# Performance work log

Hardware: AMD Instinct MI355X
Metric: run time of the kernel (lower is better)

## Reference

```python
import jax, jax.numpy as jnp
import numpy as np

# Synthetic layered DAG: 8 node-layers of width N -> 7 masked dense layers.
B = 4096        # batch
N = 2048        # nodes per DAG layer (= in_features = out_features)
DEPTH = 7       # number of weight layers (len(L) - 1)
DENSITY = 0.25  # fraction of predecessor edges present (mask sparsity)


def setup_inputs() -> dict:
    key = jax.random.key(0)
    kx, kw, km = jax.random.split(key, 3)
    x = jax.random.normal(kx, (B, N), dtype=jnp.float32)
    # Mask M: [DEPTH, N+1, N]; random 0/1 edges, last row (bias) all ones.
    m = (jax.random.uniform(km, (DEPTH, N + 1, N)) < DENSITY).astype(jnp.float32)
    M = m.at[:, -1, :].set(1.0)
    # Kaiming-uniform per column: bound = 1/sqrt(nnz_j) (torch code's init),
    # nonzero only at masked positions (W initialized to zeros elsewhere).
    nnz = jnp.maximum(M.sum(axis=1, keepdims=True), 1.0)  # [DEPTH,1,N]
    u = jax.random.uniform(kw, (DEPTH, N + 1, N), minval=-1.0, maxval=1.0)
    W = (u / jnp.sqrt(nnz)) * M
    return {"x": x, "W": W, "M": M}


def reference(x, W, M):
    # activations buffer semantics collapse to a per-layer chain because each
    # layer's preds are exactly the previous DAG layer; sinks = last layer.
    def step(acts, wm):
        w, m = wm  # [N+1, N] each
        h = jnp.concatenate(
            [acts, jnp.ones((acts.shape[0], 1), acts.dtype)], axis=1)  # [B, N+1]
        acts = jax.nn.relu(h @ (m * w))  # masked dense matmul + ReLU
        return acts, None

    out, _ = jax.lax.scan(step, x, (W, M))
    return out  # [B, N] activations of sink nodes
```

## Files before the change

### kernel.cpp

```cpp
#include <hip/hip_runtime.h>
#include <hip/hip_bf16.h>

typedef __bf16 bf16_t;
typedef __bf16 v8bf __attribute__((ext_vector_type(8)));
typedef __bf16 v4bf __attribute__((ext_vector_type(4)));
typedef float  v4f  __attribute__((ext_vector_type(4)));

#define B_ROWS 4096
#define N_COLS 2048
#define K_FULL 2049
#define K_PAD  2112
#define DEPTH  7

#define BM 128
#define BN 128
#define BK 64
#define NT (K_PAD / BK)

__global__ __launch_bounds__(256) void wt_kernel(const float* __restrict__ W,
                                                 bf16_t* __restrict__ Wt) {
  __shared__ float t[64][65];
  const int l  = blockIdx.z;
  const int k0 = blockIdx.x * 64;
  const int n0 = blockIdx.y * 64;
  const int tid = threadIdx.x;
  const int r  = tid >> 4;
  const int c4 = (tid & 15) * 4;
  const float* Wl = W + (size_t)l * K_FULL * N_COLS;
#pragma unroll
  for (int it = 0; it < 4; ++it) {
    const int k = k0 + r + it * 16;
    float4 v = make_float4(0.f, 0.f, 0.f, 0.f);
    if (k < K_FULL) v = *(const float4*)&Wl[(size_t)k * N_COLS + n0 + c4];
    t[c4 + 0][r + it * 16] = v.x;
    t[c4 + 1][r + it * 16] = v.y;
    t[c4 + 2][r + it * 16] = v.z;
    t[c4 + 3][r + it * 16] = v.w;
  }
  __syncthreads();
  bf16_t* Wtl = Wt + (size_t)l * N_COLS * K_PAD;
#pragma unroll
  for (int it = 0; it < 4; ++it) {
    const int n = r + it * 16;
    v4bf o;
    o[0] = (bf16_t)t[n][c4 + 0];
    o[1] = (bf16_t)t[n][c4 + 1];
    o[2] = (bf16_t)t[n][c4 + 2];
    o[3] = (bf16_t)t[n][c4 + 3];
    *(v4bf*)&Wtl[(size_t)(n0 + n) * K_PAD + k0 + c4] = o;
  }
}

__global__ __launch_bounds__(256) void init_kernel(const float* __restrict__ x,
                                                   bf16_t* __restrict__ A0,
                                                   bf16_t* __restrict__ A1) {
  const int c4 = (blockIdx.x * 256 + threadIdx.x) * 4;
  const int r  = blockIdx.y;
  if (c4 >= K_PAD) return;
  v4bf o;
  if (c4 < N_COLS) {
    const float4 v = *(const float4*)&x[(size_t)r * N_COLS + c4];
    o[0] = (bf16_t)v.x; o[1] = (bf16_t)v.y; o[2] = (bf16_t)v.z; o[3] = (bf16_t)v.w;
  } else {
    o[0] = (bf16_t)(c4 == N_COLS ? 1.0f : 0.0f);
    o[1] = (bf16_t)0.0f; o[2] = (bf16_t)0.0f; o[3] = (bf16_t)0.0f;
  }
  *(v4bf*)&A0[(size_t)r * K_PAD + c4] = o;
  if (c4 >= N_COLS) *(v4bf*)&A1[(size_t)r * K_PAD + c4] = o;
}

__global__ __launch_bounds__(512, 4) void gemm_kernel(
    const bf16_t* __restrict__ A, const bf16_t* __restrict__ Bt,
    bf16_t* __restrict__ Cn, float* __restrict__ Co) {
  __shared__ __align__(16) bf16_t As[BM * BK];
  __shared__ __align__(16) bf16_t Bs[BN * BK];

  const int tid  = threadIdx.x;
  const int wave = tid >> 6;
  const int lane = tid & 63;
  const int m0 = blockIdx.y * BM;
  const int n0 = blockIdx.x * BN;
  const int wm = (wave & 1) * 64;
  const int wn = (wave >> 1) * 32;
  const int quad = lane >> 4;
  const int l16  = lane & 15;

  int srow[2], scol[2];
#pragma unroll
  for (int c = 0; c < 2; ++c) {
    const int gran = wave * 128 + c * 64 + lane;
    srow[c] = gran >> 3;
    scol[c] = ((gran & 7) ^ (srow[c] & 7)) << 3;
  }
  const size_t aoff[2] = {(size_t)(m0 + srow[0]) * K_PAD + scol[0],
                          (size_t)(m0 + srow[1]) * K_PAD + scol[1]};
  const size_t boff[2] = {(size_t)(n0 + srow[0]) * K_PAD + scol[0],
                          (size_t)(n0 + srow[1]) * K_PAD + scol[1]};

  v4f acc[4][2] = {};

  for (int kt = 0; kt < NT; ++kt) {
    const int kbase = kt * BK;
    __syncthreads();
#pragma unroll
    for (int c = 0; c < 2; ++c) {
      __builtin_amdgcn_global_load_lds(
          (const __attribute__((address_space(1))) void*)(A + aoff[c] + kbase),
          (__attribute__((address_space(3))) void*)((char*)As + wave * 2048 + c * 1024),
          16, 0, 0);
    }
#pragma unroll
    for (int c = 0; c < 2; ++c) {
      __builtin_amdgcn_global_load_lds(
          (const __attribute__((address_space(1))) void*)(Bt + boff[c] + kbase),
          (__attribute__((address_space(3))) void*)((char*)Bs + wave * 2048 + c * 1024),
          16, 0, 0);
    }
    __syncthreads();

#pragma unroll
    for (int ks = 0; ks < 2; ++ks) {
      v8bf af[4], bfr[2];
      const int kg = ks * 4 + quad;
#pragma unroll
      for (int i = 0; i < 4; ++i) {
        const int arow = wm + i * 16 + l16;
        af[i] = *(const v8bf*)&As[arow * BK + ((kg ^ (arow & 7)) << 3)];
      }
#pragma unroll
      for (int j = 0; j < 2; ++j) {
        const int brow = wn + j * 16 + l16;
        bfr[j] = *(const v8bf*)&Bs[brow * BK + ((kg ^ (brow & 7)) << 3)];
      }
#pragma unroll
      for (int i = 0; i < 4; ++i)
#pragma unroll
        for (int j = 0; j < 2; ++j)
          acc[i][j] = __builtin_amdgcn_mfma_f32_16x16x32_bf16(af[i], bfr[j],
                                                              acc[i][j], 0, 0, 0);
    }
  }

#pragma unroll
  for (int i = 0; i < 4; ++i) {
#pragma unroll
    for (int j = 0; j < 2; ++j) {
#pragma unroll
      for (int r = 0; r < 4; ++r) {
        float v = acc[i][j][r];
        v = v > 0.0f ? v : 0.0f;
        const int row = m0 + wm + i * 16 + quad * 4 + r;
        const int col = n0 + wn + j * 16 + l16;
        if (Co) Co[(size_t)row * N_COLS + col] = v;
        else    Cn[(size_t)row * K_PAD + col] = (bf16_t)v;
      }
    }
  }
}

extern "C" void kernel_launch(void* const* d_in, const int* in_sizes, int n_in,
                              void* d_out, int out_size, void* d_ws, size_t ws_size,
                              hipStream_t stream) {
  const float* x = (const float*)d_in[0];
  const float* W = (const float*)d_in[1];
  float* out = (float*)d_out;

  char* ws = (char*)d_ws;
  const size_t wtBytes = (size_t)DEPTH * N_COLS * K_PAD * sizeof(bf16_t);
  const size_t aBytes  = (size_t)B_ROWS * K_PAD * sizeof(bf16_t);
  bf16_t* Wt = (bf16_t*)ws;
  bf16_t* A0 = (bf16_t*)(ws + wtBytes);
  bf16_t* A1 = (bf16_t*)(ws + wtBytes + aBytes);

  wt_kernel<<<dim3(K_PAD / 64, N_COLS / 64, DEPTH), 256, 0, stream>>>(W, Wt);
  init_kernel<<<dim3((K_PAD / 4 + 255) / 256, B_ROWS), 256, 0, stream>>>(x, A0, A1);

  bf16_t* bufs[2] = {A0, A1};
  for (int l = 0; l < DEPTH; ++l) {
    const bf16_t* Ain = bufs[l & 1];
    bf16_t* Aout      = bufs[(l + 1) & 1];
    const bf16_t* Bl  = Wt + (size_t)l * N_COLS * K_PAD;
    const bool last   = (l == DEPTH - 1);
    gemm_kernel<<<dim3(N_COLS / BN, B_ROWS / BM), 512, 0, stream>>>(
        Ain, Bl, last ? nullptr : Aout, last ? out : nullptr);
  }
}
```

Measured before the change: 517.7 us.

## Pre-swizzle weights into MFMA fragment layout and load B directly to registers

The weight transpose kernel now writes B in a fragment-major layout matching the MFMA operand order, so each lane can load its B fragments with a direct coalesced global load instead of staging through LDS. The GEMM drops the B shared-memory tile and moves from 8 waves of 64x32 to 4 waves of 64x64, doubling the accumulators per wave. This cuts LDS traffic and shared memory use per block, but B loads are now issued from global memory in the main loop without LDS reuse across waves. Register pressure also rises and the block has fewer waves.

```diff
diff --git a/kernel.cpp b/kernel.cpp
--- a/kernel.cpp
+++ b/kernel.cpp
@@ -18,10 +18,11 @@
 #define NT (K_PAD / BK)
 
 __global__ __launch_bounds__(256) void wt_kernel(const float* __restrict__ W,
-                                                 bf16_t* __restrict__ Wt) {
+                                                 bf16_t* __restrict__ Bf) {
   __shared__ float t[64][65];
   const int l  = blockIdx.z;
-  const int k0 = blockIdx.x * 64;
+  const int kt = blockIdx.x;
+  const int k0 = kt * 64;
   const int n0 = blockIdx.y * 64;
   const int tid = threadIdx.x;
   const int r  = tid >> 4;
@@ -38,16 +39,23 @@
     t[c4 + 3][r + it * 16] = v.w;
   }
   __syncthreads();
-  bf16_t* Wtl = Wt + (size_t)l * N_COLS * K_PAD;
+  bf16_t* Bfl = Bf + (size_t)l * N_COLS * K_PAD;
 #pragma unroll
-  for (int it = 0; it < 4; ++it) {
-    const int n = r + it * 16;
-    v4bf o;
-    o[0] = (bf16_t)t[n][c4 + 0];
-    o[1] = (bf16_t)t[n][c4 + 1];
-    o[2] = (bf16_t)t[n][c4 + 2];
-    o[3] = (bf16_t)t[n][c4 + 3];
-    *(v4bf*)&Wtl[(size_t)(n0 + n) * K_PAD + k0 + c4] = o;
+  for (int half = 0; half < 2; ++half) {
+    const int u    = half * 256 + tid;
+    const int ks   = u >> 8;
+    const int ngl  = (u >> 6) & 3;
+    const int lane = u & 63;
+    const int quad = lane >> 4;
+    const int l16  = lane & 15;
+    const int nl   = ngl * 16 + l16;
+    const int kl   = ks * 32 + quad * 8;
+    v8bf o;
+#pragma unroll
+    for (int e = 0; e < 8; ++e) o[e] = (bf16_t)t[nl][kl + e];
+    const size_t idx =
+        ((((size_t)kt * 2 + ks) * 128 + (n0 >> 4) + ngl) * 64 + lane) * 8;
+    *(v8bf*)&Bfl[idx] = o;
   }
 }
 
@@ -69,11 +77,10 @@
   if (c4 >= N_COLS) *(v4bf*)&A1[(size_t)r * K_PAD + c4] = o;
 }
 
-__global__ __launch_bounds__(512, 4) void gemm_kernel(
-    const bf16_t* __restrict__ A, const bf16_t* __restrict__ Bt,
+__global__ __launch_bounds__(256, 2) void gemm_kernel(
+    const bf16_t* __restrict__ A, const bf16_t* __restrict__ Bf,
     bf16_t* __restrict__ Cn, float* __restrict__ Co) {
   __shared__ __align__(16) bf16_t As[BM * BK];
-  __shared__ __align__(16) bf16_t Bs[BN * BK];
 
   const int tid  = threadIdx.x;
   const int wave = tid >> 6;
@@ -81,46 +88,48 @@
   const int m0 = blockIdx.y * BM;
   const int n0 = blockIdx.x * BN;
   const int wm = (wave & 1) * 64;
-  const int wn = (wave >> 1) * 32;
+  const int wn = (wave >> 1) * 64;
   const int quad = lane >> 4;
   const int l16  = lane & 15;
+  const int ngbase = (n0 >> 4) + (wn >> 4);
 
-  int srow[2], scol[2];
+  int srow[4], scol[4];
 #pragma unroll
-  for (int c = 0; c < 2; ++c) {
-    const int gran = wave * 128 + c * 64 + lane;
+  for (int c = 0; c < 4; ++c) {
+    const int gran = wave * 256 + c * 64 + lane;
     srow[c] = gran >> 3;
     scol[c] = ((gran & 7) ^ (srow[c] & 7)) << 3;
   }
-  const size_t aoff[2] = {(size_t)(m0 + srow[0]) * K_PAD + scol[0],
-                          (size_t)(m0 + srow[1]) * K_PAD + scol[1]};
-  const size_t boff[2] = {(size_t)(n0 + srow[0]) * K_PAD + scol[0],
-                          (size_t)(n0 + srow[1]) * K_PAD + scol[1]};
+  size_t aoff[4];
+#pragma unroll
+  for (int c = 0; c < 4; ++c) aoff[c] = (size_t)(m0 + srow[c]) * K_PAD + scol[c];
 
-  v4f acc[4][2] = {};
+  v4f acc[4][4] = {};
 
   for (int kt = 0; kt < NT; ++kt) {
     const int kbase = kt * BK;
     __syncthreads();
+
+    v8bf bfr[2][4];
 #pragma unroll
-    for (int c = 0; c < 2; ++c) {
+    for (int ks = 0; ks < 2; ++ks)
+#pragma unroll
+      for (int j = 0; j < 4; ++j)
+        bfr[ks][j] = *(const v8bf*)&Bf[((((size_t)kt * 2 + ks) * 128 +
+                                        ngbase + j) * 64 + lane) * 8];
+
+#pragma unroll
+    for (int c = 0; c < 4; ++c) {
       __builtin_amdgcn_global_load_lds(
           (const __attribute__((address_space(1))) void*)(A + aoff[c] + kbase),
-          (__attribute__((address_space(3))) void*)((char*)As + wave * 2048 + c * 1024),
-          16, 0, 0);
-    }
-#pragma unroll
-    for (int c = 0; c < 2; ++c) {
-      __builtin_amdgcn_global_load_lds(
-          (const __attribute__((address_space(1))) void*)(Bt + boff[c] + kbase),
-          (__attribute__((address_space(3))) void*)((char*)Bs + wave * 2048 + c * 1024),
+          (__attribute__((address_space(3))) void*)((char*)As + wave * 4096 + c * 1024),
           16, 0, 0);
     }
     __syncthreads();
 
 #pragma unroll
     for (int ks = 0; ks < 2; ++ks) {
-      v8bf af[4], bfr[2];
+      v8bf af[4];
       const int kg = ks * 4 + quad;
 #pragma unroll
       for (int i = 0; i < 4; ++i) {
@@ -128,15 +137,10 @@
         af[i] = *(const v8bf*)&As[arow * BK + ((kg ^ (arow & 7)) << 3)];
       }
 #pragma unroll
-      for (int j = 0; j < 2; ++j) {
-        const int brow = wn + j * 16 + l16;
-        bfr[j] = *(const v8bf*)&Bs[brow * BK + ((kg ^ (brow & 7)) << 3)];
-      }
-#pragma unroll
       for (int i = 0; i < 4; ++i)
 #pragma unroll
-        for (int j = 0; j < 2; ++j)
-          acc[i][j] = __builtin_amdgcn_mfma_f32_16x16x32_bf16(af[i], bfr[j],
+        for (int j = 0; j < 4; ++j)
+          acc[i][j] = __builtin_amdgcn_mfma_f32_16x16x32_bf16(af[i], bfr[ks][j],
                                                               acc[i][j], 0, 0, 0);
     }
   }
@@ -144,7 +148,7 @@
 #pragma unroll
   for (int i = 0; i < 4; ++i) {
 #pragma unroll
-    for (int j = 0; j < 2; ++j) {
+    for (int j = 0; j < 4; ++j) {
 #pragma unroll
       for (int r = 0; r < 4; ++r) {
         float v = acc[i][j][r];
@@ -166,22 +170,22 @@
   float* out = (float*)d_out;
 
   char* ws = (char*)d_ws;
-  const size_t wtBytes = (size_t)DEPTH * N_COLS * K_PAD * sizeof(bf16_t);
+  const size_t bfBytes = (size_t)DEPTH * N_COLS * K_PAD * sizeof(bf16_t);
   const size_t aBytes  = (size_t)B_ROWS * K_PAD * sizeof(bf16_t);
-  bf16_t* Wt = (bf16_t*)ws;
-  bf16_t* A0 = (bf16_t*)(ws + wtBytes);
-  bf16_t* A1 = (bf16_t*)(ws + wtBytes + aBytes);
+  bf16_t* Bf = (bf16_t*)ws;
+  bf16_t* A0 = (bf16_t*)(ws + bfBytes);
+  bf16_t* A1 = (bf16_t*)(ws + bfBytes + aBytes);
 
-  wt_kernel<<<dim3(K_PAD / 64, N_COLS / 64, DEPTH), 256, 0, stream>>>(W, Wt);
+  wt_kernel<<<dim3(NT, N_COLS / 64, DEPTH), 256, 0, stream>>>(W, Bf);
   init_kernel<<<dim3((K_PAD / 4 + 255) / 256, B_ROWS), 256, 0, stream>>>(x, A0, A1);
 
   bf16_t* bufs[2] = {A0, A1};
   for (int l = 0; l < DEPTH; ++l) {
     const bf16_t* Ain = bufs[l & 1];
     bf16_t* Aout      = bufs[(l + 1) & 1];
-    const bf16_t* Bl  = Wt + (size_t)l * N_COLS * K_PAD;
+    const bf16_t* Bl  = Bf + (size_t)l * N_COLS * K_PAD;
     const bool last   = (l == DEPTH - 1);
-    gemm_kernel<<<dim3(N_COLS / BN, B_ROWS / BM), 512, 0, stream>>>(
+    gemm_kernel<<<dim3(N_COLS / BN, B_ROWS / BM), 256, 0, stream>>>(
         Ain, Bl, last ? nullptr : Aout, last ? out : nullptr);
   }
 }
```

Result: slower. 531.1 us (+2.6%).
